# Optimization experiments

Hardware: AMD Instinct MI355X
Metric: run time of the kernel (lower is better)

The kernel has to match this reference:

```python
import jax, jax.numpy as jnp
import numpy as np

N_EMBED = 512
E_DIM = 256
BETA = 0.25


def setup_inputs() -> dict:
    key = jax.random.key(0)
    k1, k2 = jax.random.split(key)
    z = jax.random.normal(k1, (32, 16, 16, 16, E_DIM), dtype=jnp.float32)
    embedding = jax.random.normal(k2, (N_EMBED, E_DIM), dtype=jnp.float32)
    return {"z": z, "embedding": embedding}


def reference(z, embedding):
    # Flatten spatial/batch dims: [N, e_dim]
    zf = z.reshape(-1, E_DIM)
    # similarity = ||z||^2 + ||e||^2 - 2 z.e  (squared distances)
    sim = (
        jnp.sum(zf * zf, axis=1, keepdims=True)
        + jnp.sum(embedding * embedding, axis=1)
        - 2.0 * jnp.einsum("bd,nd->bn", zf, embedding)
    )
    # NOTE: original code uses argmax (farthest code) -- faithfully reproduced.
    codebook_idxs = jnp.argmax(sim, axis=-1)
    # histogram side-effect: codebook_hist[idx] += 1
    hist = jnp.zeros((N_EMBED,), dtype=jnp.float32).at[codebook_idxs].add(1.0)
    z_q = embedding[codebook_idxs].reshape(z.shape)
    vq_loss = jnp.mean((z_q - jax.lax.stop_gradient(z)) ** 2)
    commitment_loss = BETA * jnp.mean((jax.lax.stop_gradient(z_q) - z) ** 2)
    # straight-through estimator
    z_q_st = z + jax.lax.stop_gradient(z_q - z)
    return (z_q_st, vq_loss, commitment_loss, codebook_idxs, hist)
```

## Files before the change

### kernel.cpp

```cpp
#include <hip/hip_runtime.h>
#include <hip/hip_bf16.h>

#define D 256
#define NC 512
#define NROWS 131072L

#define OFF_ZQ   0L
#define OFF_VQ   33554432L
#define OFF_CM   33554433L
#define OFF_IDX  33554434L
#define OFF_HIST 33685506L

#define WS_LPART 0
#define WS_HIST  2048
#define WS_E2    2560
#define WS_CNT   3072
#define WS_AMB   3136
#define WS_FIDX  134208
#define WS_BK    265280
#define WS_NEED  (330816L * 4)

#define MARGIN 1.25f

typedef __attribute__((ext_vector_type(8))) short bf16x8;
typedef __attribute__((ext_vector_type(4))) float f32x4;

#define AS1 __attribute__((address_space(1)))
#define AS3 __attribute__((address_space(3)))

__device__ __forceinline__ unsigned short f2bf(float f) {
    union { float f; unsigned int u; } a; a.f = f;
    return (unsigned short)((a.u + 0x7FFFu + ((a.u >> 16) & 1u)) >> 16);
}

__global__ void vq_e2(const float* __restrict__ e, float* __restrict__ e2) {
    int c = blockIdx.x;
    int l = threadIdx.x;
    float4 v = *(const float4*)(e + c * D + l * 4);
    float s = v.x * v.x + v.y * v.y + v.z * v.z + v.w * v.w;
    #pragma unroll
    for (int off = 32; off; off >>= 1) s += __shfl_xor(s, off);
    if (l == 0) e2[c] = s;
}

__global__ void vq_convB(const float* __restrict__ e, unsigned short* __restrict__ Bk,
                         float* __restrict__ e2, float* __restrict__ hist,
                         int* __restrict__ acnt) {
    __shared__ float r4[4];
    int code = blockIdx.x, k = threadIdx.x;
    float v = e[code * D + k];
    Bk[((k >> 5) * NC + code) * 32 + (k & 31)] = f2bf(v);
    float s = v * v;
    #pragma unroll
    for (int off = 32; off; off >>= 1) s += __shfl_xor(s, off);
    if ((k & 63) == 0) r4[k >> 6] = s;
    if (k == 0) {
        hist[code] = 0.0f;
        if (code == 0) *acnt = 0;
    }
    __syncthreads();
    if (k == 0) e2[code] = r4[0] + r4[1] + r4[2] + r4[3];
}

__global__ __launch_bounds__(512, 3)
void vq_gemm(const float* __restrict__ z, const unsigned short* __restrict__ Bk,
             const float* __restrict__ e2, int* __restrict__ fidx,
             int* __restrict__ acnt, int* __restrict__ alist) {
    __shared__ __align__(16) unsigned short zh[64 * 264];
    __shared__ float red[64 * 25];

    const int tid = threadIdx.x;
    const int w = tid >> 6, l = tid & 63, q = l >> 4, ln = l & 15;
    const long row0 = (long)blockIdx.x * 64;

    const unsigned short* bbase = Bk + ((w * 64 + ln) * 32 + q * 8);
    bf16x8 bnx[4];
    #pragma unroll
    for (int nt = 0; nt < 4; ++nt)
        bnx[nt] = *(const bf16x8*)(bbase + nt * (16 * 32));

    #pragma unroll
    for (int j = 0; j < 8; ++j) {
        int c = j * 512 + tid;
        int row = c >> 6, c4 = (c & 63) * 4;
        float4 av = *(const float4*)(z + (row0 + row) * D + c4);
        *(ushort4*)&zh[row * 264 + c4] =
            make_ushort4(f2bf(av.x), f2bf(av.y), f2bf(av.z), f2bf(av.w));
    }
    __syncthreads();

    const unsigned short* abase = &zh[ln * 264 + q * 8];

    f32x4 acc[4][4];
    #pragma unroll
    for (int mt = 0; mt < 4; ++mt)
        #pragma unroll
        for (int nt = 0; nt < 4; ++nt) acc[mt][nt] = (f32x4){0.f, 0.f, 0.f, 0.f};

    #pragma unroll
    for (int s = 0; s < 8; ++s) {
        bf16x8 bcur[4], af[4];
        #pragma unroll
        for (int nt = 0; nt < 4; ++nt) bcur[nt] = bnx[nt];
        if (s < 7) {
            const unsigned short* bs = bbase + (s + 1) * (NC * 32);
            #pragma unroll
            for (int nt = 0; nt < 4; ++nt)
                bnx[nt] = *(const bf16x8*)(bs + nt * (16 * 32));
        }
        #pragma unroll
        for (int mt = 0; mt < 4; ++mt)
            af[mt] = *(const bf16x8*)(abase + mt * (16 * 264) + s * 32);
        #pragma unroll
        for (int mt = 0; mt < 4; ++mt)
            #pragma unroll
            for (int nt = 0; nt < 4; ++nt)
                acc[mt][nt] = __builtin_amdgcn_mfma_f32_16x16x32_bf16(af[mt], bcur[nt], acc[mt][nt], 0, 0, 0);
    }

    float e2v[4];
    #pragma unroll
    for (int nt = 0; nt < 4; ++nt) e2v[nt] = e2[w * 64 + nt * 16 + ln];

    #pragma unroll
    for (int mt = 0; mt < 4; ++mt) {
        #pragma unroll
        for (int r = 0; r < 4; ++r) {
            float v1 = -3.0e38f, v2 = -3.0e38f; int i1 = 0;
            #pragma unroll
            for (int nt = 0; nt < 4; ++nt) {
                float v = fmaf(-2.0f, acc[mt][nt][r], e2v[nt]);
                int c = w * 64 + nt * 16 + ln;
                if (v > v1) { v2 = v1; v1 = v; i1 = c; }
                else v2 = fmaxf(v2, v);
            }
            float v1p = v1;
            #pragma unroll
            for (int off = 1; off < 16; off <<= 1) {
                float ov1 = __shfl_xor(v1, off);
                float ov2 = __shfl_xor(v2, off);
                v2 = fmaxf(fmaxf(v2, ov2), fminf(v1, ov1));
                v1 = fmaxf(v1, ov1);
            }
            unsigned long long mm = __ballot(v1p == v1);
            unsigned int gm = (unsigned int)((mm >> (q * 16)) & 0xFFFFULL);
            int src = q * 16 + (__ffs(gm) - 1);
            i1 = __shfl(i1, src);
            if (ln == 0) {
                int rr = mt * 16 + q * 4 + r;
                red[rr * 25 + w * 3 + 0] = v1;
                red[rr * 25 + w * 3 + 1] = (float)i1;
                red[rr * 25 + w * 3 + 2] = v2;
            }
        }
    }
    __syncthreads();
    if (tid < 64) {
        float v1 = -3.0e38f, v2 = -3.0e38f; int i1 = 0;
        #pragma unroll
        for (int g = 0; g < 8; ++g) {
            float rv1 = red[tid * 25 + g * 3 + 0];
            int   ri  = (int)red[tid * 25 + g * 3 + 1];
            float rv2 = red[tid * 25 + g * 3 + 2];
            if (rv1 > v1) { v2 = fmaxf(v1, rv2); v1 = rv1; i1 = ri; }
            else v2 = fmaxf(v2, rv1);
        }
        fidx[row0 + tid] = i1;
        int amb = (v1 - v2 < MARGIN) ? 1 : 0;
        unsigned long long m = __ballot(amb);
        int nb = __popcll(m);
        int basep = 0;
        if (tid == 0 && nb) basep = atomicAdd(acnt, nb);
        basep = __shfl(basep, 0);
        if (amb) {
            int pfx = __popcll(m & ((1ULL << tid) - 1ULL));
            alist[basep + pfx] = (int)(row0 + tid);
        }
    }
}

__global__ __launch_bounds__(256, 2)
void vq_refine(const float* __restrict__ z, const float* __restrict__ e,
               const float* __restrict__ e2, const int* __restrict__ acnt,
               const int* __restrict__ alist, int* __restrict__ fidx) {
    __shared__ __align__(16) float z_s[32][D];
    __shared__ __align__(16) float e_s[16][NC + 4];
    __shared__ int rowg[32];
    __shared__ int idx_s[32];
    const int tid = threadIdx.x, lane = tid & 63, w = tid >> 6;
    const int cnt = *acnt;
    for (int g = blockIdx.x; g * 32 < cnt; g += gridDim.x) {
        const int base = g * 32;
        __syncthreads();
        if (tid < 32) rowg[tid] = alist[min(base + tid, cnt - 1)];
        __syncthreads();
        #pragma unroll
        for (int j = 0; j < 8; ++j) {
            int c = j * 256 + tid, rl = c >> 6, c4 = (c & 63) * 4;
            *(float4*)&z_s[rl][c4] = *(const float4*)(z + (long)rowg[rl] * D + c4);
        }
        float acc[8][8];
        #pragma unroll
        for (int r = 0; r < 8; ++r)
            #pragma unroll
            for (int c = 0; c < 8; ++c) acc[r][c] = 0.0f;
        const int r0 = w * 8, c_lo = lane * 4;
        for (int kc = 0; kc < D; kc += 16) {
            __syncthreads();
            #pragma unroll
            for (int p = 0; p < 8; ++p) {
                int c = p * 64 + (tid >> 2), kk4 = (tid & 3) * 4;
                float4 v = *(const float4*)(e + c * D + kc + kk4);
                e_s[kk4 + 0][c] = v.x; e_s[kk4 + 1][c] = v.y;
                e_s[kk4 + 2][c] = v.z; e_s[kk4 + 3][c] = v.w;
            }
            __syncthreads();
            #pragma unroll
            for (int k4 = 0; k4 < 16; k4 += 4) {
                float zr[8][4];
                #pragma unroll
                for (int r = 0; r < 8; ++r) *(float4*)zr[r] = *(const float4*)&z_s[r0 + r][kc + k4];
                #pragma unroll
                for (int kk = 0; kk < 4; ++kk) {
                    float ev[8];
                    *(float4*)&ev[0] = *(const float4*)&e_s[k4 + kk][c_lo];
                    *(float4*)&ev[4] = *(const float4*)&e_s[k4 + kk][c_lo + 256];
                    #pragma unroll
                    for (int r = 0; r < 8; ++r)
                        #pragma unroll
                        for (int c = 0; c < 8; ++c) acc[r][c] = fmaf(zr[r][kk], ev[c], acc[r][c]);
                }
            }
        }
        float e2v[8];
        #pragma unroll
        for (int gg = 0; gg < 2; ++gg)
            #pragma unroll
            for (int i = 0; i < 4; ++i) e2v[gg * 4 + i] = e2[gg * 256 + c_lo + i];
        #pragma unroll
        for (int r = 0; r < 8; ++r) {
            float bvv = -3.0e38f; int bc = 0;
            #pragma unroll
            for (int c = 0; c < 8; ++c) {
                int col = (c >> 2) * 256 + c_lo + (c & 3);
                float v = e2v[c] - 2.0f * acc[r][c];
                if (v > bvv) { bvv = v; bc = col; }
            }
            #pragma unroll
            for (int off = 32; off; off >>= 1) {
                float ov = __shfl_xor(bvv, off); int oc = __shfl_xor(bc, off);
                if (ov > bvv || (ov == bvv && oc < bc)) { bvv = ov; bc = oc; }
            }
            if (lane == 0) idx_s[r0 + r] = bc;
        }
        __syncthreads();
        if (tid < 32 && base + tid < cnt) fidx[rowg[tid]] = idx_s[tid];
    }
}

__global__ __launch_bounds__(256)
void vq_hist(const int* __restrict__ fidx, float* __restrict__ hist) {
    __shared__ int h[NC];
    const int t = threadIdx.x;
    h[t] = 0; h[t + 256] = 0;
    __syncthreads();
    const long base = (long)blockIdx.x * 2048;
    #pragma unroll
    for (int j = 0; j < 8; ++j) {
        long i = base + j * 256 + t;
        atomicAdd(&h[fidx[i]], 1);
    }
    __syncthreads();
    #pragma unroll
    for (int j = 0; j < 2; ++j) {
        int k = j * 256 + t;
        int c = h[k];
        if (c) atomicAdd(&hist[k], (float)c);
    }
}

__global__ __launch_bounds__(256)
void vq_epi(const float* __restrict__ z, const float* __restrict__ e,
            const int* __restrict__ fidx, float* __restrict__ out,
            float* __restrict__ lpart) {
    __shared__ int idxs[64];
    __shared__ float rs[4];
    const int t = threadIdx.x, lane = t & 63, w = t >> 6;
    const long row0 = (long)blockIdx.x * 64;
    if (t < 64) {
        int ix = fidx[row0 + t];
        idxs[t] = ix;
        out[OFF_IDX + row0 + t] = (float)ix;
    }
    __syncthreads();
    float ls = 0.f;
    #pragma unroll 4
    for (int j = 0; j < 16; ++j) {
        const int r = w * 16 + j;
        const long row = row0 + r;
        const int idx = idxs[r];
        float4 zv = *(const float4*)(z + row * D + lane * 4);
        float4 ev = *(const float4*)(e + (long)idx * D + lane * 4);
        float4 dq;
        dq.x = ev.x - zv.x; dq.y = ev.y - zv.y; dq.z = ev.z - zv.z; dq.w = ev.w - zv.w;
        float4 o;
        o.x = zv.x + dq.x; o.y = zv.y + dq.y; o.z = zv.z + dq.z; o.w = zv.w + dq.w;
        *(float4*)(out + OFF_ZQ + row * D + lane * 4) = o;
        ls += dq.x * dq.x + dq.y * dq.y + dq.z * dq.z + dq.w * dq.w;
    }
    #pragma unroll
    for (int off = 32; off; off >>= 1) ls += __shfl_xor(ls, off);
    if (lane == 0) rs[w] = ls;
    __syncthreads();
    if (t == 0) lpart[blockIdx.x] = rs[0] + rs[1] + rs[2] + rs[3];
}

__global__ void vq_fin(const float* __restrict__ ws, float* __restrict__ out) {
    __shared__ float sred[16];
    const int t = threadIdx.x, lane = t & 63, w = t >> 6;
    float s = ws[WS_LPART + t] + ws[WS_LPART + t + 1024];
    #pragma unroll
    for (int off = 32; off; off >>= 1) s += __shfl_xor(s, off);
    if (lane == 0) sred[w] = s;
    __syncthreads();
    if (t == 0) {
        float tot = 0.f;
        #pragma unroll
        for (int i = 0; i < 16; ++i) tot += sred[i];
        float m = tot / 33554432.0f;
        out[OFF_VQ] = m;
        out[OFF_CM] = 0.25f * m;
    }
    if (t < NC) out[OFF_HIST + t] = ws[WS_HIST + t];
}

__global__ __launch_bounds__(256, 2)
void vq_main_fb(const float* __restrict__ z, const float* __restrict__ e,
                const float* __restrict__ e2, float* __restrict__ out,
                float* __restrict__ ws_loss, float* __restrict__ ws_hist) {
    __shared__ __align__(16) float z_s[32][D];
    __shared__ __align__(16) float e_s[16][NC + 4];
    __shared__ int   idx_s[32];
    __shared__ float red_s[4];
    const int tid = threadIdx.x, lane = tid & 63, w = tid >> 6;
    const long row0 = (long)blockIdx.x * 32;
    {
        const float4* zg = (const float4*)(z + row0 * D);
        float4* zs = (float4*)(&z_s[0][0]);
        #pragma unroll
        for (int i = 0; i < 8; ++i) zs[i * 256 + tid] = zg[i * 256 + tid];
    }
    float acc[8][8];
    #pragma unroll
    for (int r = 0; r < 8; ++r)
        #pragma unroll
        for (int c = 0; c < 8; ++c) acc[r][c] = 0.0f;
    const int r0 = w * 8, c_lo = lane * 4;
    for (int kc = 0; kc < D; kc += 16) {
        __syncthreads();
        #pragma unroll
        for (int p = 0; p < 8; ++p) {
            int c = p * 64 + (tid >> 2), kk4 = (tid & 3) * 4;
            float4 v = *(const float4*)(e + c * D + kc + kk4);
            e_s[kk4 + 0][c] = v.x; e_s[kk4 + 1][c] = v.y;
            e_s[kk4 + 2][c] = v.z; e_s[kk4 + 3][c] = v.w;
        }
        __syncthreads();
        #pragma unroll
        for (int k4 = 0; k4 < 16; k4 += 4) {
            float zr[8][4];
            #pragma unroll
            for (int r = 0; r < 8; ++r) *(float4*)zr[r] = *(const float4*)&z_s[r0 + r][kc + k4];
            #pragma unroll
            for (int kk = 0; kk < 4; ++kk) {
                float ev[8];
                *(float4*)&ev[0] = *(const float4*)&e_s[k4 + kk][c_lo];
                *(float4*)&ev[4] = *(const float4*)&e_s[k4 + kk][c_lo + 256];
                #pragma unroll
                for (int r = 0; r < 8; ++r)
                    #pragma unroll
                    for (int c = 0; c < 8; ++c) acc[r][c] = fmaf(zr[r][kk], ev[c], acc[r][c]);
            }
        }
    }
    float e2v[8];
    #pragma unroll
    for (int g = 0; g < 2; ++g)
        #pragma unroll
        for (int i = 0; i < 4; ++i) e2v[g * 4 + i] = e2[g * 256 + c_lo + i];
    #pragma unroll
    for (int r = 0; r < 8; ++r) {
        float bvv = -3.0e38f; int bc = 0;
        #pragma unroll
        for (int c = 0; c < 8; ++c) {
            int col = (c >> 2) * 256 + c_lo + (c & 3);
            float v = e2v[c] - 2.0f * acc[r][c];
            if (v > bvv) { bvv = v; bc = col; }
        }
        #pragma unroll
        for (int off = 32; off; off >>= 1) {
            float ov = __shfl_xor(bvv, off); int oc = __shfl_xor(bc, off);
            if (ov > bvv || (ov == bvv && oc < bc)) { bvv = ov; bc = oc; }
        }
        if (lane == 0) idx_s[r] = bc;
    }
    __syncthreads();
    if (tid < 32) {
        int bc = idx_s[tid];
        out[OFF_IDX + row0 + tid] = (float)bc;
        atomicAdd(&ws_hist[bc], 1.0f);
    }
    float lsum = 0.0f;
    for (int r = 0; r < 32; ++r) {
        int idx = idx_s[r];
        float ev = e[idx * D + tid];
        float zv = z_s[r][tid];
        float dq = ev - zv;
        out[OFF_ZQ + (row0 + r) * D + tid] = zv + dq;
        lsum += dq * dq;
    }
    #pragma unroll
    for (int off = 32; off; off >>= 1) lsum += __shfl_xor(lsum, off);
    if (lane == 0) red_s[w] = lsum;
    __syncthreads();
    if (tid == 0) atomicAdd(ws_loss, red_s[0] + red_s[1] + red_s[2] + red_s[3]);
}

__global__ void vq_init_fb(float* __restrict__ ws) {
    int t = threadIdx.x;
    if (t < 513) ws[t] = 0.0f;
}
__global__ void vq_fin_fb(const float* __restrict__ ws, float* __restrict__ out) {
    int t = blockIdx.x * blockDim.x + threadIdx.x;
    if (t < NC) out[OFF_HIST + t] = ws[1 + t];
    if (t == NC) {
        float m = ws[0] / 33554432.0f;
        out[OFF_VQ] = m; out[OFF_CM] = 0.25f * m;
    }
}

extern "C" void kernel_launch(void* const* d_in, const int* in_sizes, int n_in,
                              void* d_out, int out_size, void* d_ws, size_t ws_size,
                              hipStream_t stream) {
    const float* z = (const float*)d_in[0];
    const float* e = (const float*)d_in[1];
    float* out = (float*)d_out;
    float* ws  = (float*)d_ws;

    if (ws_size >= (size_t)WS_NEED) {
        float* lpart = ws + WS_LPART;
        float* hist  = ws + WS_HIST;
        float* e2    = ws + WS_E2;
        int*   acnt  = (int*)(ws + WS_CNT);
        int*   alist = (int*)(ws + WS_AMB);
        int*   fidx  = (int*)(ws + WS_FIDX);
        unsigned short* Bk = (unsigned short*)(ws + WS_BK);

        vq_convB<<<NC, 256, 0, stream>>>(e, Bk, e2, hist, acnt);
        vq_gemm<<<2048, 512, 0, stream>>>(z, Bk, e2, fidx, acnt, alist);
        vq_refine<<<512, 256, 0, stream>>>(z, e, e2, acnt, alist, fidx);
        vq_hist<<<64, 256, 0, stream>>>(fidx, hist);
        vq_epi<<<2048, 256, 0, stream>>>(z, e, fidx, out, lpart);
        vq_fin<<<1, 1024, 0, stream>>>(ws, out);
    } else {
        float* ws_loss = ws;
        float* ws_hist = ws + 1;
        float* ws_e2   = ws + 513;
        vq_init_fb<<<1, 1024, 0, stream>>>(ws);
        vq_e2<<<NC, 64, 0, stream>>>(e, ws_e2);
        vq_main_fb<<<4096, 256, 0, stream>>>(z, e, ws_e2, out, ws_loss, ws_hist);
        vq_fin_fb<<<3, 256, 0, stream>>>(ws, out);
    }
}
```

Before: 395.3 us.

## Restructure VQ GEMM per column tile with streaming argmax and tighter margin

The GEMM loop now runs over one 16-column tile at a time, with 4 accumulators instead of 16. It folds each tile into running top-2 values per row, so fewer registers stay live at once. B fragments stream through a 4-deep register ring, A fragments are reloaded from shared memory for each tile, and launch bounds rise to 4 blocks per CU. The bf16 ambiguity margin also shrinks from 1.25 to 0.75, so fewer rows go to the exact fp32 refine pass, at some risk of missing true argmax ties caused by bf16 error.

```diff
diff --git a/kernel.cpp b/kernel.cpp
--- a/kernel.cpp
+++ b/kernel.cpp
@@ -20,13 +20,10 @@
 #define WS_BK    265280
 #define WS_NEED  (330816L * 4)
 
-#define MARGIN 1.25f
+#define MARGIN 0.75f
 
 typedef __attribute__((ext_vector_type(8))) short bf16x8;
 typedef __attribute__((ext_vector_type(4))) float f32x4;
-
-#define AS1 __attribute__((address_space(1)))
-#define AS3 __attribute__((address_space(3)))
 
 __device__ __forceinline__ unsigned short f2bf(float f) {
     union { float f; unsigned int u; } a; a.f = f;
@@ -62,7 +59,7 @@
     if (k == 0) e2[code] = r4[0] + r4[1] + r4[2] + r4[3];
 }
 
-__global__ __launch_bounds__(512, 3)
+__global__ __launch_bounds__(512, 4)
 void vq_gemm(const float* __restrict__ z, const unsigned short* __restrict__ Bk,
              const float* __restrict__ e2, int* __restrict__ fidx,
              int* __restrict__ acnt, int* __restrict__ alist) {
@@ -72,12 +69,6 @@
     const int tid = threadIdx.x;
     const int w = tid >> 6, l = tid & 63, q = l >> 4, ln = l & 15;
     const long row0 = (long)blockIdx.x * 64;
-
-    const unsigned short* bbase = Bk + ((w * 64 + ln) * 32 + q * 8);
-    bf16x8 bnx[4];
-    #pragma unroll
-    for (int nt = 0; nt < 4; ++nt)
-        bnx[nt] = *(const bf16x8*)(bbase + nt * (16 * 32));
 
     #pragma unroll
     for (int j = 0; j < 8; ++j) {
@@ -87,86 +78,86 @@
         *(ushort4*)&zh[row * 264 + c4] =
             make_ushort4(f2bf(av.x), f2bf(av.y), f2bf(av.z), f2bf(av.w));
     }
-    __syncthreads();
-
-    const unsigned short* abase = &zh[ln * 264 + q * 8];
-
-    f32x4 acc[4][4];
-    #pragma unroll
-    for (int mt = 0; mt < 4; ++mt)
-        #pragma unroll
-        for (int nt = 0; nt < 4; ++nt) acc[mt][nt] = (f32x4){0.f, 0.f, 0.f, 0.f};
-
-    #pragma unroll
-    for (int s = 0; s < 8; ++s) {
-        bf16x8 bcur[4], af[4];
-        #pragma unroll
-        for (int nt = 0; nt < 4; ++nt) bcur[nt] = bnx[nt];
-        if (s < 7) {
-            const unsigned short* bs = bbase + (s + 1) * (NC * 32);
-            #pragma unroll
-            for (int nt = 0; nt < 4; ++nt)
-                bnx[nt] = *(const bf16x8*)(bs + nt * (16 * 32));
+
+    const unsigned short* bb = Bk + ((w * 64 + ln) * 32 + q * 8);
+    bf16x8 ring[4];
+    #pragma unroll
+    for (int p = 0; p < 4; ++p)
+        ring[p] = *(const bf16x8*)(bb + (p & 7) * (NC * 32) + (p >> 3) * (16 * 32));
+
+    __syncthreads();
+
+    float v1[16], v2[16]; int i1[16];
+    #pragma unroll
+    for (int k = 0; k < 16; ++k) { v1[k] = -3.0e38f; v2[k] = -3.0e38f; i1[k] = 0; }
+
+    #pragma unroll
+    for (int nt = 0; nt < 4; ++nt) {
+        const int colc = w * 64 + nt * 16 + ln;
+        const float e2v = e2[colc];
+        f32x4 acc[4];
+        #pragma unroll
+        for (int mt = 0; mt < 4; ++mt) acc[mt] = (f32x4){0.f, 0.f, 0.f, 0.f};
+        #pragma unroll
+        for (int s = 0; s < 8; ++s) {
+            const int it = nt * 8 + s;
+            bf16x8 b = ring[it & 3];
+            if (it + 4 < 32) {
+                const int jt = it + 4;
+                ring[it & 3] = *(const bf16x8*)(bb + (jt & 7) * (NC * 32) + (jt >> 3) * (16 * 32));
+            }
+            #pragma unroll
+            for (int mt = 0; mt < 4; ++mt) {
+                bf16x8 a = *(const bf16x8*)&zh[(mt * 16 + ln) * 264 + s * 32 + q * 8];
+                acc[mt] = __builtin_amdgcn_mfma_f32_16x16x32_bf16(a, b, acc[mt], 0, 0, 0);
+            }
         }
         #pragma unroll
         for (int mt = 0; mt < 4; ++mt)
-            af[mt] = *(const bf16x8*)(abase + mt * (16 * 264) + s * 32);
-        #pragma unroll
-        for (int mt = 0; mt < 4; ++mt)
-            #pragma unroll
-            for (int nt = 0; nt < 4; ++nt)
-                acc[mt][nt] = __builtin_amdgcn_mfma_f32_16x16x32_bf16(af[mt], bcur[nt], acc[mt][nt], 0, 0, 0);
-    }
-
-    float e2v[4];
-    #pragma unroll
-    for (int nt = 0; nt < 4; ++nt) e2v[nt] = e2[w * 64 + nt * 16 + ln];
-
-    #pragma unroll
-    for (int mt = 0; mt < 4; ++mt) {
-        #pragma unroll
-        for (int r = 0; r < 4; ++r) {
-            float v1 = -3.0e38f, v2 = -3.0e38f; int i1 = 0;
-            #pragma unroll
-            for (int nt = 0; nt < 4; ++nt) {
-                float v = fmaf(-2.0f, acc[mt][nt][r], e2v[nt]);
-                int c = w * 64 + nt * 16 + ln;
-                if (v > v1) { v2 = v1; v1 = v; i1 = c; }
-                else v2 = fmaxf(v2, v);
-            }
-            float v1p = v1;
-            #pragma unroll
-            for (int off = 1; off < 16; off <<= 1) {
-                float ov1 = __shfl_xor(v1, off);
-                float ov2 = __shfl_xor(v2, off);
-                v2 = fmaxf(fmaxf(v2, ov2), fminf(v1, ov1));
-                v1 = fmaxf(v1, ov1);
-            }
-            unsigned long long mm = __ballot(v1p == v1);
-            unsigned int gm = (unsigned int)((mm >> (q * 16)) & 0xFFFFULL);
-            int src = q * 16 + (__ffs(gm) - 1);
-            i1 = __shfl(i1, src);
-            if (ln == 0) {
-                int rr = mt * 16 + q * 4 + r;
-                red[rr * 25 + w * 3 + 0] = v1;
-                red[rr * 25 + w * 3 + 1] = (float)i1;
-                red[rr * 25 + w * 3 + 2] = v2;
-            }
+            #pragma unroll
+            for (int r = 0; r < 4; ++r) {
+                const int k = mt * 4 + r;
+                float v = fmaf(-2.0f, acc[mt][r], e2v);
+                if (v > v1[k]) { v2[k] = v1[k]; v1[k] = v; i1[k] = colc; }
+                else v2[k] = fmaxf(v2[k], v);
+            }
+    }
+
+    #pragma unroll
+    for (int k = 0; k < 16; ++k) {
+        float v1p = v1[k];
+        #pragma unroll
+        for (int off = 1; off < 16; off <<= 1) {
+            float o1 = __shfl_xor(v1[k], off);
+            float o2 = __shfl_xor(v2[k], off);
+            v2[k] = fmaxf(fmaxf(v2[k], o2), fminf(v1[k], o1));
+            v1[k] = fmaxf(v1[k], o1);
+        }
+        unsigned long long mm = __ballot(v1p == v1[k]);
+        unsigned int gm = (unsigned int)((mm >> (q * 16)) & 0xFFFFULL);
+        int src = (q << 4) + (__ffs(gm) - 1);
+        int ii = __shfl(i1[k], src);
+        if (ln == 0) {
+            const int mt = k >> 2, r = k & 3;
+            const int rr = mt * 16 + q * 4 + r;
+            red[rr * 25 + w * 3 + 0] = v1[k];
+            red[rr * 25 + w * 3 + 1] = (float)ii;
+            red[rr * 25 + w * 3 + 2] = v2[k];
         }
     }
     __syncthreads();
     if (tid < 64) {
-        float v1 = -3.0e38f, v2 = -3.0e38f; int i1 = 0;
+        float v1m = -3.0e38f, v2m = -3.0e38f; int i1m = 0;
         #pragma unroll
         for (int g = 0; g < 8; ++g) {
             float rv1 = red[tid * 25 + g * 3 + 0];
             int   ri  = (int)red[tid * 25 + g * 3 + 1];
             float rv2 = red[tid * 25 + g * 3 + 2];
-            if (rv1 > v1) { v2 = fmaxf(v1, rv2); v1 = rv1; i1 = ri; }
-            else v2 = fmaxf(v2, rv1);
-        }
-        fidx[row0 + tid] = i1;
-        int amb = (v1 - v2 < MARGIN) ? 1 : 0;
+            if (rv1 > v1m) { v2m = fmaxf(v1m, rv2); v1m = rv1; i1m = ri; }
+            else v2m = fmaxf(v2m, rv1);
+        }
+        fidx[row0 + tid] = i1m;
+        int amb = (v1m - v2m < MARGIN) ? 1 : 0;
         unsigned long long m = __ballot(amb);
         int nb = __popcll(m);
         int basep = 0;
```

Measured after the change: 382.6 us. -3.2%, faster.
